# Performance work log

Measured on AMD Instinct MI355X. Metric: run time of the kernel, lower is better.

## Reference

```python
import jax, jax.numpy as jnp
import numpy as np

B, S, H, HF, V, L, NB, K = 8, 512, 1024, 512, 32000, 4, 8, 2
EPS = 1e-5


def _ln(x, g, b):
    m = jnp.mean(x, -1, keepdims=True)
    v = jnp.mean((x - m) ** 2, -1, keepdims=True)
    return (x - m) * jax.lax.rsqrt(v + EPS) * g + b


def setup_inputs() -> dict:
    key = jax.random.key(0)
    ks = jax.random.split(key, 12)
    n = lambda i, shape, s=0.02: jax.random.normal(ks[i], shape, jnp.float32) * s
    return {
        "input_ids": jax.random.randint(ks[0], (B, S), 0, V),
        "emb": n(1, (V, H)),
        "pos": n(2, (1, 512, H)),
        "torsion_field": jnp.zeros((1, H), jnp.float32),
        "lm_w": n(3, (H, V)),
        "lm_b": jnp.zeros((V,), jnp.float32),
        "sel_w": n(4, (L, H, NB)),
        "sel_b": jnp.zeros((L, NB), jnp.float32),
        "g1": jnp.ones((L, NB, H), jnp.float32),
        "b1": jnp.zeros((L, NB, H), jnp.float32),
        "attn_w": n(5, (L, NB, H, H)),
        "attn_b": jnp.zeros((L, NB, H), jnp.float32),
        "g2": jnp.ones((L, NB, H), jnp.float32),
        "b2": jnp.zeros((L, NB, H), jnp.float32),
        "ff1_w": n(6, (L, NB, H, HF)),
        "ff1_b": jnp.zeros((L, NB, HF), jnp.float32),
        "ff2_w": n(7, (L, NB, HF, H)),
        "ff2_b": jnp.zeros((L, NB, H), jnp.float32),
        "tg": n(8, (L, NB, H), 0.01),
    }


def _forward(input_ids, emb, pos, torsion_field, lm_w, lm_b, sel_w, sel_b,
             g1, b1, attn_w, attn_b, g2, b2, ff1_w, ff1_b, ff2_w, ff2_b, tg):
    # embedding + positional encoding
    h = emb[input_ids] + pos[:, :input_ids.shape[1], :]        # [B,S,H]
    tf = torsion_field[0]                                      # [H] (zeros buffer)
    PRIORITY = 0.5  # fresh block: success_rate*0.6 + excitement*0.4 = 0.5
    for l in range(L):
        # router: sigmoid(Linear(mean-pooled x)), mixed with block priority; topk on batch row 0
        scores = jax.nn.sigmoid(jnp.mean(h, 1) @ sel_w[l] + sel_b[l])   # [B,NB]
        adj0 = scores[0] * 0.7 + PRIORITY * 0.3                         # [NB]
        _, top_idx = jax.lax.top_k(adj0, K)                             # [K]
        params = jax.tree_util.tree_map(
            lambda p: p[l][top_idx],
            (g1, b1, attn_w, attn_b, g2, b2, ff1_w, ff1_b, ff2_w, ff2_b, tg))

        def blk(carry, p):
            pg1, pb1, pwa, pba, pg2, pb2, pw1, pbf1, pw2, pbf2, ptg = p
            x = carry
            ha = _ln(x, pg1, pb1) @ pwa + pba                           # [B,S,H]
            ha = ha * (1.0 + jax.nn.sigmoid(ptg) * tf)[None, None, :]
            hm = x + 0.5 * ha
            h2 = _ln(hm, pg2, pb2)
            h2 = jax.nn.gelu(h2 @ pw1 + pbf1, approximate=False) @ pw2 + pbf2
            return hm + 0.5 * h2, None

        h, _ = jax.lax.scan(blk, h, params)
        h = 1.5 * h  # h*0.5 + h after each layer
    return h @ lm_w + lm_b                                     # [B,S,V]


def reference(input_ids, emb, pos, torsion_field, lm_w, lm_b, sel_w, sel_b,
              g1, b1, attn_w, attn_b, g2, b2, ff1_w, ff1_b, ff2_w, ff2_b, tg):
    return _forward(input_ids, emb, pos, torsion_field, lm_w, lm_b, sel_w, sel_b,
                    g1, b1, attn_w, attn_b, g2, b2, ff1_w, ff1_b, ff2_w, ff2_b, tg)
```

## Files before the change

kernel.cpp:

```cpp
#include <hip/hip_runtime.h>


typedef unsigned short u16;
typedef short bf16x8 __attribute__((ext_vector_type(8)));
typedef float f32x4 __attribute__((ext_vector_type(4)));

struct __align__(8) u16x4_t { u16 x, y, z, w; };

#define MTOT 4096
#define HDIM 1024
#define HFF  512
#define VOC  32000
#define NLAYER 4
#define NBLK 8

#define VMW(n) asm volatile("s_waitcnt vmcnt(" #n ")" ::: "memory")
#define BARR() do { asm volatile("" ::: "memory"); __builtin_amdgcn_s_barrier(); asm volatile("" ::: "memory"); } while (0)

__device__ __forceinline__ u16 f2bf(float f) {
  unsigned u = __float_as_uint(f);
  unsigned r = u + 0x7FFFu + ((u >> 16) & 1u);
  return (u16)(r >> 16);
}

__device__ __forceinline__ float sigmoidf_(float z) {
  return 1.0f / (1.0f + expf(-z));
}

__device__ __forceinline__ void gload16(const void* g, void* l) {
  __builtin_amdgcn_global_load_lds(
      (const __attribute__((address_space(1))) void*)g,
      (__attribute__((address_space(3))) void*)l, 16, 0, 0);
}

__global__ void embed_lm_kernel(const int* __restrict__ ids,
                                const float* __restrict__ emb,
                                const float* __restrict__ pos,
                                float* __restrict__ x,
                                const float* __restrict__ lm_w,
                                u16* __restrict__ lmT) {
  __shared__ float tile[32][33];
  int b = blockIdx.x, tid = threadIdx.x;
  if (b < MTOT) {
    int s = b & 511;
    int id = ids[b];
    float4 e = ((const float4*)(emb + (size_t)id * HDIM))[tid];
    float4 p = ((const float4*)(pos + (size_t)s * HDIM))[tid];
    float4 r;
    r.x = e.x + p.x; r.y = e.y + p.y; r.z = e.z + p.z; r.w = e.w + p.w;
    ((float4*)(x + (size_t)b * HDIM))[tid] = r;
    return;
  }
  int c = b - MTOT;
  int n0 = (c % 1000) * 32, k0 = (c / 1000) * 32;
  int tx = tid & 31, ty = tid >> 5;
#pragma unroll
  for (int j = 0; j < 4; ++j) {
    int kr = k0 + ty + j * 8;
    tile[ty + j * 8][tx] = lm_w[(size_t)kr * VOC + n0 + tx];
  }
  __syncthreads();
#pragma unroll
  for (int j = 0; j < 4; ++j) {
    int nr = n0 + ty + j * 8;
    lmT[(size_t)nr * HDIM + k0 + tx] = f2bf(tile[tx][ty + j * 8]);
  }
}

__global__ void colsum_kernel(const float* __restrict__ x, float* __restrict__ partial) {
  int j = blockIdx.x;
  int t = threadIdx.x;
  float4 s; s.x = 0.f; s.y = 0.f; s.z = 0.f; s.w = 0.f;
  for (int r = 0; r < 8; ++r) {
    float4 a = ((const float4*)(x + (size_t)(j * 8 + r) * HDIM))[t];
    s.x += a.x; s.y += a.y; s.z += a.z; s.w += a.w;
  }
  ((float4*)(partial + (size_t)j * HDIM))[t] = s;
}

__global__ void router_finalize(const float* __restrict__ partial,
                                const float* __restrict__ selw,
                                const float* __restrict__ selb,
                                const float* __restrict__ tg_l,
                                const float* __restrict__ tf,
                                int* __restrict__ idx_out,
                                float* __restrict__ scale_out) {
  int t = threadIdx.x;
  float s = 0.f;
  for (int j = 0; j < 64; ++j) s += partial[(size_t)j * HDIM + t];
  float mean = s * (1.0f / 512.0f);
  __shared__ float sm[HDIM];
  __shared__ float sc[NBLK];
  __shared__ int sidx[2];
  sm[t] = mean;
  __syncthreads();
  int wave = t >> 6, lane = t & 63;
  if (wave < NBLK) {
    float p = 0.f;
    for (int h = lane; h < HDIM; h += 64) p += sm[h] * selw[h * NBLK + wave];
    for (int o = 32; o; o >>= 1) p += __shfl_down(p, o);
    if (lane == 0) sc[wave] = p;
  }
  __syncthreads();
  if (t == 0) {
    float adj[NBLK];
    for (int i = 0; i < NBLK; ++i) {
      float z = sc[i] + selb[i];
      adj[i] = sigmoidf_(z) * 0.7f + 0.15f;
    }
    int i0 = 0;
    for (int i = 1; i < NBLK; ++i) if (adj[i] > adj[i0]) i0 = i;
    int i1 = -1;
    for (int i = 0; i < NBLK; ++i) {
      if (i == i0) continue;
      if (i1 < 0 || adj[i] > adj[i1]) i1 = i;
    }
    idx_out[0] = i0; idx_out[1] = i1;
    sidx[0] = i0; sidx[1] = i1;
  }
  __syncthreads();
  for (int k = 0; k < 2; ++k) {
    int id = sidx[k];
    float z = tg_l[(size_t)id * HDIM + t];
    scale_out[k * HDIM + t] = 1.0f + sigmoidf_(z) * tf[t];
  }
}

__global__ void prep_kernel(const float* __restrict__ aw,
                            const float* __restrict__ f1w,
                            const float* __restrict__ f2w,
                            const int* __restrict__ idx, int slot,
                            u16* __restrict__ wA, u16* __restrict__ w1,
                            u16* __restrict__ w2,
                            const float* __restrict__ x,
                            const float* __restrict__ g_base,
                            const float* __restrict__ b_base,
                            u16* __restrict__ abf) {
  __shared__ float sh[32 * 33];
  int b = blockIdx.x, tid = threadIdx.x;
  int id = idx[slot];
  if (b < 2048) {
    float (*tile)[33] = (float(*)[33])sh;
    const float* src; u16* dst; int K, N, n0, k0;
    if (b < 1024) {
      K = 1024; N = 1024; src = aw + (size_t)id * 1024 * 1024;
      n0 = (b & 31) * 32; k0 = (b >> 5) * 32; dst = wA;
    } else if (b < 1536) {
      int c = b - 1024; K = 1024; N = 512; src = f1w + (size_t)id * 1024 * 512;
      n0 = (c & 15) * 32; k0 = (c >> 4) * 32; dst = w1;
    } else {
      int c = b - 1536; K = 512; N = 1024; src = f2w + (size_t)id * 512 * 1024;
      n0 = (c & 31) * 32; k0 = (c >> 5) * 32; dst = w2;
    }
    int tx = tid & 31, ty = tid >> 5;
#pragma unroll
    for (int j = 0; j < 4; ++j) {
      int kr = k0 + ty + j * 8;
      tile[ty + j * 8][tx] = src[(size_t)kr * N + n0 + tx];
    }
    __syncthreads();
#pragma unroll
    for (int j = 0; j < 4; ++j) {
      int nr = n0 + ty + j * 8;
      dst[(size_t)nr * K + k0 + tx] = f2bf(tile[tx][ty + j * 8]);
    }
    return;
  }
  int row = b - 2048, t = tid;
  const float* g = g_base + (size_t)id * HDIM;
  const float* bb = b_base + (size_t)id * HDIM;
  float4 v = ((const float4*)(x + (size_t)row * HDIM))[t];
  float s = v.x + v.y + v.z + v.w;
  float q = v.x * v.x + v.y * v.y + v.z * v.z + v.w * v.w;
  for (int o = 32; o; o >>= 1) { s += __shfl_down(s, o); q += __shfl_down(q, o); }
  float* ss = sh; float* sq = sh + 8;
  int wave = t >> 6, lane = t & 63;
  if (lane == 0) { ss[wave] = s; sq[wave] = q; }
  __syncthreads();
  if (t == 0) {
    float S = ss[0] + ss[1] + ss[2] + ss[3];
    float Q = sq[0] + sq[1] + sq[2] + sq[3];
    ss[0] = S * (1.0f / 1024.0f);
    sq[0] = Q * (1.0f / 1024.0f);
  }
  __syncthreads();
  float mean = ss[0];
  float var = sq[0] - mean * mean;
  float rs = rsqrtf(var + 1e-5f);
  float4 gv = ((const float4*)g)[t];
  float4 bv = ((const float4*)bb)[t];
  u16x4_t o4;
  o4.x = f2bf((v.x - mean) * rs * gv.x + bv.x);
  o4.y = f2bf((v.y - mean) * rs * gv.y + bv.y);
  o4.z = f2bf((v.z - mean) * rs * gv.z + bv.z);
  o4.w = f2bf((v.w - mean) * rs * gv.w + bv.w);
  ((u16x4_t*)(abf + (size_t)row * HDIM))[t] = o4;
}

__global__ void ln_kernel(const float* __restrict__ x,
                          const float* __restrict__ g_base,
                          const float* __restrict__ b_base,
                          const int* __restrict__ idx_ptr, int slot,
                          u16* __restrict__ out) {
  int row = blockIdx.x, t = threadIdx.x;
  size_t off = (size_t)idx_ptr[slot] * HDIM;
  const float* g = g_base + off;
  const float* b = b_base + off;
  float4 v = ((const float4*)(x + (size_t)row * HDIM))[t];
  float s = v.x + v.y + v.z + v.w;
  float q = v.x * v.x + v.y * v.y + v.z * v.z + v.w * v.w;
  for (int o = 32; o; o >>= 1) { s += __shfl_down(s, o); q += __shfl_down(q, o); }
  __shared__ float ss[4], sq[4];
  int wave = t >> 6, lane = t & 63;
  if (lane == 0) { ss[wave] = s; sq[wave] = q; }
  __syncthreads();
  if (t == 0) {
    float S = ss[0] + ss[1] + ss[2] + ss[3];
    float Q = sq[0] + sq[1] + sq[2] + sq[3];
    ss[0] = S * (1.0f / 1024.0f);
    sq[0] = Q * (1.0f / 1024.0f);
  }
  __syncthreads();
  float mean = ss[0];
  float var = sq[0] - mean * mean;
  float rs = rsqrtf(var + 1e-5f);
  float4 gv = ((const float4*)g)[t];
  float4 bv = ((const float4*)b)[t];
  u16x4_t o4;
  o4.x = f2bf((v.x - mean) * rs * gv.x + bv.x);
  o4.y = f2bf((v.y - mean) * rs * gv.y + bv.y);
  o4.z = f2bf((v.z - mean) * rs * gv.z + bv.z);
  o4.w = f2bf((v.w - mean) * rs * gv.w + bv.w);
  ((u16x4_t*)(out + (size_t)row * HDIM))[t] = o4;
}

template <int BM, int BN, int EPI>
__global__ __launch_bounds__(256) void gemm_layer(
    const u16* __restrict__ A, const u16* __restrict__ Bt, int N, int K,
    const float* __restrict__ bias_base, const int* __restrict__ idx_ptr,
    int slot, int bias_stride, const float* __restrict__ scale,
    float* __restrict__ xres, u16* __restrict__ outb, float lscale) {
  constexpr int TM = BM / 2, TN = BN / 2;
  constexpr int FM = TM / 16, FN = TN / 16;
  constexpr int NLD = (BM + BN) / 32;
  __shared__ __align__(16) u16 lds[(BM + BN) * 64];

  const int tid = threadIdx.x, wave = tid >> 6, lane = tid & 63;
  const int m0 = blockIdx.y * BM, n0 = blockIdx.x * BN;
  const int wm = wave >> 1, wn = wave & 1;
  const int fr = lane & 15, g = lane >> 4;
  const float* bias =
      bias_base + (idx_ptr ? (size_t)idx_ptr[slot] * bias_stride : 0);

  const u16* gbase[NLD];
  unsigned ldsoff[NLD];
#pragma unroll
  for (int j = 0; j < NLD; ++j) {
    int lo = (tid + j * 256) * 16;
    int q = (lo >> 4) & 7;
    if (lo < BM * 128) {
      int row = lo >> 7;
      gbase[j] = A + (size_t)(m0 + row) * K + (q ^ (row & 7)) * 8;
    } else {
      int bo = lo - BM * 128;
      int row = bo >> 7;
      gbase[j] = Bt + (size_t)(n0 + row) * K + (q ^ (row & 7)) * 8;
    }
    ldsoff[j] = (unsigned)(lo >> 1);
  }

  unsigned offA[FM][2], offB[FN][2];
#pragma unroll
  for (int mi = 0; mi < FM; ++mi)
#pragma unroll
    for (int kk = 0; kk < 2; ++kk)
      offA[mi][kk] = (unsigned)((wm * TM + mi * 16 + fr) * 128 +
                                (((kk * 4 + g) ^ (fr & 7)) << 4));
#pragma unroll
  for (int ni = 0; ni < FN; ++ni)
#pragma unroll
    for (int kk = 0; kk < 2; ++kk)
      offB[ni][kk] = (unsigned)(BM * 128 + (wn * TN + ni * 16 + fr) * 128 +
                                (((kk * 4 + g) ^ (fr & 7)) << 4));

  f32x4 acc[FM][FN];
#pragma unroll
  for (int i = 0; i < FM; ++i)
#pragma unroll
    for (int j = 0; j < FN; ++j) acc[i][j] = (f32x4){0.f, 0.f, 0.f, 0.f};

  for (int kt = 0; kt < K; kt += 64) {
#pragma unroll
    for (int j = 0; j < NLD; ++j) gload16(gbase[j] + kt, lds + ldsoff[j]);
    __syncthreads();
#pragma unroll
    for (int kk = 0; kk < 2; ++kk) {
      bf16x8 af[FM], bf[FN];
#pragma unroll
      for (int mi = 0; mi < FM; ++mi)
        af[mi] = *(const bf16x8*)((const char*)lds + offA[mi][kk]);
#pragma unroll
      for (int ni = 0; ni < FN; ++ni)
        bf[ni] = *(const bf16x8*)((const char*)lds + offB[ni][kk]);
#pragma unroll
      for (int mi = 0; mi < FM; ++mi)
#pragma unroll
        for (int ni = 0; ni < FN; ++ni)
          acc[mi][ni] = __builtin_amdgcn_mfma_f32_16x16x32_bf16(
              af[mi], bf[ni], acc[mi][ni], 0, 0, 0);
    }
    __syncthreads();
  }

  const int rb = g * 4, cn = fr;
  float bvv[FN], svv[FN];
#pragma unroll
  for (int ni = 0; ni < FN; ++ni) {
    int n = n0 + wn * TN + ni * 16 + cn;
    bvv[ni] = bias[n];
    svv[ni] = (EPI == 0) ? scale[n] : 0.f;
  }
#pragma unroll
  for (int mi = 0; mi < FM; ++mi) {
#pragma unroll
    for (int r = 0; r < 4; ++r) {
      int m = m0 + wm * TM + mi * 16 + rb + r;
      size_t base = (size_t)m * N + n0 + wn * TN + cn;
#pragma unroll
      for (int ni = 0; ni < FN; ++ni) {
        float c = acc[mi][ni][r] + bvv[ni];
        size_t o = base + ni * 16;
        if (EPI == 0) {
          xres[o] = xres[o] + 0.5f * (c * svv[ni]);
        } else if (EPI == 1) {
          float ge = 0.5f * c * (1.0f + erff(c * 0.70710678118654752f));
          outb[o] = f2bf(ge);
        } else if (EPI == 2) {
          xres[o] = (xres[o] + 0.5f * c) * lscale;
        } else {
          float v = (xres[o] + 0.5f * c) * lscale;
          xres[o] = v;
          outb[o] = f2bf(v);
        }
      }
    }
  }
}

__global__ __launch_bounds__(512, 2) void gemm_lm(
    const u16* __restrict__ A, const u16* __restrict__ Bt,
    const float* __restrict__ bias, float* __restrict__ out) {
  constexpr int K = HDIM;
  constexpr int N = VOC;
  constexpr int NT = K / 64;
  __shared__ __align__(16) u16 smbuf[2 * 32768];

  const int tid = threadIdx.x, wid = tid >> 6, lane = tid & 63;
  const int bid = blockIdx.x;
  const int vbid = (bid & 7) * 250 + (bid >> 3);
  const int n0 = (vbid >> 4) * 256;
  const int m0 = (vbid & 15) * 256;
  const int wm = wid >> 2, wn = wid & 3;
  const int fr = lane & 15, g = lane >> 4;

  const int r0 = tid >> 3, q = tid & 7;
  const int sg = (q ^ (r0 & 7)) * 8;
  const u16* usrc[4][2];
  unsigned uoff[4][2];
  usrc[0][0] = Bt + (size_t)(n0 + r0) * K + sg;        uoff[0][0] = 16384u + tid * 8;
  usrc[0][1] = Bt + (size_t)(n0 + 64 + r0) * K + sg;   uoff[0][1] = 20480u + tid * 8;
  usrc[1][0] = Bt + (size_t)(n0 + 128 + r0) * K + sg;  uoff[1][0] = 24576u + tid * 8;
  usrc[1][1] = Bt + (size_t)(n0 + 192 + r0) * K + sg;  uoff[1][1] = 28672u + tid * 8;
  usrc[2][0] = A + (size_t)(m0 + r0) * K + sg;         uoff[2][0] = 0u + tid * 8;
  usrc[2][1] = A + (size_t)(m0 + 128 + r0) * K + sg;   uoff[2][1] = 8192u + tid * 8;
  usrc[3][0] = A + (size_t)(m0 + 64 + r0) * K + sg;    uoff[3][0] = 4096u + tid * 8;
  usrc[3][1] = A + (size_t)(m0 + 192 + r0) * K + sg;   uoff[3][1] = 12288u + tid * 8;

  unsigned offA[8][2], offB[4][2];
#pragma unroll
  for (int mi = 0; mi < 8; ++mi)
#pragma unroll
    for (int kk = 0; kk < 2; ++kk)
      offA[mi][kk] = (unsigned)((wm * 128 + mi * 16 + fr) * 128 +
                                (((kk * 4 + g) ^ (fr & 7)) << 4));
#pragma unroll
  for (int ni = 0; ni < 4; ++ni)
#pragma unroll
    for (int kk = 0; kk < 2; ++kk)
      offB[ni][kk] = (unsigned)(32768 + (wn * 64 + ni * 16 + fr) * 128 +
                                (((kk * 4 + g) ^ (fr & 7)) << 4));

  f32x4 acc[8][4];
#pragma unroll
  for (int i = 0; i < 8; ++i)
#pragma unroll
    for (int j = 0; j < 4; ++j) acc[i][j] = (f32x4){0.f, 0.f, 0.f, 0.f};

#pragma unroll
  for (int u = 0; u < 4; ++u) {
    gload16(usrc[u][0], smbuf + uoff[u][0]);
    gload16(usrc[u][1], smbuf + uoff[u][1]);
  }

  for (int t = 0; t < NT; ++t) {
    const char* cb = (const char*)smbuf + (size_t)(t & 1) * 65536;
    u16* nb = smbuf + ((t + 1) & 1) * 32768;
    const int ko = (t + 1) * 64;
    const bool st = (t + 1 < NT);
    bf16x8 avl[4], avh[4], bv[4];
    VMW(2);
    BARR();
#pragma unroll
    for (int ni = 0; ni < 4; ++ni) bv[ni] = *(const bf16x8*)(cb + offB[ni][0]);
#pragma unroll
    for (int mi = 0; mi < 4; ++mi) avl[mi] = *(const bf16x8*)(cb + offA[mi][0]);
    if (st) {
      gload16(usrc[0][0] + ko, nb + uoff[0][0]);
      gload16(usrc[0][1] + ko, nb + uoff[0][1]);
    }
    __builtin_amdgcn_s_setprio(1);
#pragma unroll
    for (int mi = 0; mi < 4; ++mi)
#pragma unroll
      for (int ni = 0; ni < 4; ++ni)
        acc[mi][ni] = __builtin_amdgcn_mfma_f32_16x16x32_bf16(
            avl[mi], bv[ni], acc[mi][ni], 0, 0, 0);
    __builtin_amdgcn_s_setprio(0);
    if (t < NT - 1) { VMW(2); } else { VMW(0); }
    BARR();
#pragma unroll
    for (int mi = 0; mi < 4; ++mi)
      avh[mi] = *(const bf16x8*)(cb + offA[4 + mi][0]);
    if (st) {
      gload16(usrc[1][0] + ko, nb + uoff[1][0]);
      gload16(usrc[1][1] + ko, nb + uoff[1][1]);
    }
    __builtin_amdgcn_s_setprio(1);
#pragma unroll
    for (int mi = 0; mi < 4; ++mi)
#pragma unroll
      for (int ni = 0; ni < 4; ++ni)
        acc[4 + mi][ni] = __builtin_amdgcn_mfma_f32_16x16x32_bf16(
            avh[mi], bv[ni], acc[4 + mi][ni], 0, 0, 0);
    __builtin_amdgcn_s_setprio(0);
#pragma unroll
    for (int ni = 0; ni < 4; ++ni) bv[ni] = *(const bf16x8*)(cb + offB[ni][1]);
#pragma unroll
    for (int mi = 0; mi < 4; ++mi) avl[mi] = *(const bf16x8*)(cb + offA[mi][1]);
    if (st) {
      gload16(usrc[2][0] + ko, nb + uoff[2][0]);
      gload16(usrc[2][1] + ko, nb + uoff[2][1]);
    }
    __builtin_amdgcn_s_setprio(1);
#pragma unroll
    for (int mi = 0; mi < 4; ++mi)
#pragma unroll
      for (int ni = 0; ni < 4; ++ni)
        acc[mi][ni] = __builtin_amdgcn_mfma_f32_16x16x32_bf16(
            avl[mi], bv[ni], acc[mi][ni], 0, 0, 0);
    __builtin_amdgcn_s_setprio(0);
#pragma unroll
    for (int mi = 0; mi < 4; ++mi)
      avh[mi] = *(const bf16x8*)(cb + offA[4 + mi][1]);
    if (st) {
      gload16(usrc[3][0] + ko, nb + uoff[3][0]);
      gload16(usrc[3][1] + ko, nb + uoff[3][1]);
    }
    __builtin_amdgcn_s_setprio(1);
#pragma unroll
    for (int mi = 0; mi < 4; ++mi)
#pragma unroll
      for (int ni = 0; ni < 4; ++ni)
        acc[4 + mi][ni] = __builtin_amdgcn_mfma_f32_16x16x32_bf16(
            avh[mi], bv[ni], acc[4 + mi][ni], 0, 0, 0);
    __builtin_amdgcn_s_setprio(0);
  }

  const int rb = g * 4, cn = fr;
  float bvv[4];
#pragma unroll
  for (int ni = 0; ni < 4; ++ni) bvv[ni] = bias[n0 + wn * 64 + ni * 16 + cn];
#pragma unroll
  for (int mi = 0; mi < 8; ++mi) {
#pragma unroll
    for (int r = 0; r < 4; ++r) {
      int m = m0 + wm * 128 + mi * 16 + rb + r;
      float* orow = out + (size_t)m * N + n0 + wn * 64 + cn;
#pragma unroll
      for (int ni = 0; ni < 4; ++ni)
        __builtin_nontemporal_store(acc[mi][ni][r] + bvv[ni], orow + ni * 16);
    }
  }
}

extern "C" void kernel_launch(void* const* d_in, const int* in_sizes, int n_in,
                              void* d_out, int out_size, void* d_ws,
                              size_t ws_size, hipStream_t stream) {
  (void)in_sizes; (void)n_in; (void)out_size; (void)ws_size;
  const int*   ids    = (const int*)d_in[0];
  const float* emb    = (const float*)d_in[1];
  const float* pos    = (const float*)d_in[2];
  const float* tf     = (const float*)d_in[3];
  const float* lm_w   = (const float*)d_in[4];
  const float* lm_b   = (const float*)d_in[5];
  const float* sel_w  = (const float*)d_in[6];
  const float* sel_b  = (const float*)d_in[7];
  const float* g1     = (const float*)d_in[8];
  const float* b1     = (const float*)d_in[9];
  const float* attn_w = (const float*)d_in[10];
  const float* attn_b = (const float*)d_in[11];
  const float* g2     = (const float*)d_in[12];
  const float* b2     = (const float*)d_in[13];
  const float* ff1_w  = (const float*)d_in[14];
  const float* ff1_b  = (const float*)d_in[15];
  const float* ff2_w  = (const float*)d_in[16];
  const float* ff2_b  = (const float*)d_in[17];
  const float* tg     = (const float*)d_in[18];
  float* out = (float*)d_out;

  char* ws = (char*)d_ws;
  float* x       = (float*)(ws + 0);
  u16*   abf     = (u16*)(ws + 16777216);
  u16*   tbuf    = (u16*)(ws + 25165824);
  u16*   wA      = (u16*)(ws + 29360128);
  u16*   w1      = (u16*)(ws + 31457280);
  u16*   w2      = (u16*)(ws + 32505856);
  u16*   lmT     = (u16*)(ws + 33554432);
  float* partial = (float*)(ws + 99090432);
  float* scalev  = (float*)(ws + 99352576);
  int*   idx     = (int*)(ws + 99360768);

  embed_lm_kernel<<<MTOT + VOC, 256, 0, stream>>>(ids, emb, pos, x, lm_w, lmT);

  for (int l = 0; l < NLAYER; ++l) {
    colsum_kernel<<<64, 256, 0, stream>>>(x, partial);
    router_finalize<<<1, 1024, 0, stream>>>(
        partial, sel_w + (size_t)l * HDIM * NBLK, sel_b + l * NBLK,
        tg + (size_t)l * NBLK * HDIM, tf, idx, scalev);
    const float* aw_l  = attn_w + (size_t)l * NBLK * HDIM * HDIM;
    const float* f1w_l = ff1_w + (size_t)l * NBLK * HDIM * HFF;
    const float* f2w_l = ff2_w + (size_t)l * NBLK * HFF * HDIM;
    for (int k = 0; k < 2; ++k) {
      prep_kernel<<<2048 + MTOT, 256, 0, stream>>>(
          aw_l, f1w_l, f2w_l, idx, k, wA, w1, w2, x,
          g1 + (size_t)l * NBLK * HDIM, b1 + (size_t)l * NBLK * HDIM, abf);
      gemm_layer<128, 64, 0><<<dim3(16, 32), 256, 0, stream>>>(
          abf, wA, HDIM, HDIM, attn_b + (size_t)l * NBLK * HDIM, idx, k, HDIM,
          scalev + k * HDIM, x, nullptr, 1.0f);
      ln_kernel<<<MTOT, 256, 0, stream>>>(x, g2 + (size_t)l * NBLK * HDIM,
                                          b2 + (size_t)l * NBLK * HDIM, idx, k,
                                          abf);
      gemm_layer<64, 64, 1><<<dim3(8, 64), 256, 0, stream>>>(
          abf, w1, HFF, HDIM, ff1_b + (size_t)l * NBLK * HFF, idx, k, HFF,
          nullptr, nullptr, tbuf, 1.0f);
      float lsc = (k == 1) ? 1.5f : 1.0f;
      if (l == NLAYER - 1 && k == 1) {
        gemm_layer<128, 64, 3><<<dim3(16, 32), 256, 0, stream>>>(
            tbuf, w2, HDIM, HFF, ff2_b + (size_t)l * NBLK * HDIM, idx, k, HDIM,
            nullptr, x, abf, lsc);
      } else {
        gemm_layer<128, 64, 2><<<dim3(16, 32), 256, 0, stream>>>(
            tbuf, w2, HDIM, HFF, ff2_b + (size_t)l * NBLK * HDIM, idx, k, HDIM,
            nullptr, x, nullptr, lsc);
      }
    }
  }

  gemm_lm<<<2000, 512, 0, stream>>>(abf, lmT, lm_b, out);
}
```

Measured before the change: 977.7 us.

## Unroll LM-head GEMM K loop by two with barrier-per-quarter ping-pong schedule

Restructures the LM-head GEMM main loop to process two K tiles per iteration with fixed double-buffer addresses. It adds a barrier around every MFMA quarter so waves alternate between LDS reads plus global issue and MFMA bursts, in a ping-pong style. MFMAs are reordered so consecutive instructions use different accumulators, which reduces back-to-back dependency stalls. The cost is many more barriers per K tile, and the waitcnt placement changes, which risks synchronisation overhead or subtle correctness issues around buffer reuse.

```diff
diff --git a/kernel.cpp b/kernel.cpp
--- a/kernel.cpp
+++ b/kernel.cpp
@@ -347,12 +347,26 @@
   }
 }
 
+#define MFMA_Q(ACCBASE, AV0, AV1, AV2, AV3)                                   \
+  __builtin_amdgcn_s_setprio(1);                                              \
+  _Pragma("unroll")                                                           \
+  for (int ni = 0; ni < 4; ++ni) {                                            \
+    acc[ACCBASE + 0][ni] = __builtin_amdgcn_mfma_f32_16x16x32_bf16(           \
+        AV0, bv[ni], acc[ACCBASE + 0][ni], 0, 0, 0);                          \
+    acc[ACCBASE + 1][ni] = __builtin_amdgcn_mfma_f32_16x16x32_bf16(           \
+        AV1, bv[ni], acc[ACCBASE + 1][ni], 0, 0, 0);                          \
+    acc[ACCBASE + 2][ni] = __builtin_amdgcn_mfma_f32_16x16x32_bf16(           \
+        AV2, bv[ni], acc[ACCBASE + 2][ni], 0, 0, 0);                          \
+    acc[ACCBASE + 3][ni] = __builtin_amdgcn_mfma_f32_16x16x32_bf16(           \
+        AV3, bv[ni], acc[ACCBASE + 3][ni], 0, 0, 0);                          \
+  }                                                                           \
+  __builtin_amdgcn_s_setprio(0);
+
 __global__ __launch_bounds__(512, 2) void gemm_lm(
     const u16* __restrict__ A, const u16* __restrict__ Bt,
     const float* __restrict__ bias, float* __restrict__ out) {
   constexpr int K = HDIM;
   constexpr int N = VOC;
-  constexpr int NT = K / 64;
   __shared__ __align__(16) u16 smbuf[2 * 32768];
 
   const int tid = threadIdx.x, wid = tid >> 6, lane = tid & 63;
@@ -401,79 +415,113 @@
     gload16(usrc[u][0], smbuf + uoff[u][0]);
     gload16(usrc[u][1], smbuf + uoff[u][1]);
   }
-
-  for (int t = 0; t < NT; ++t) {
-    const char* cb = (const char*)smbuf + (size_t)(t & 1) * 65536;
-    u16* nb = smbuf + ((t + 1) & 1) * 32768;
-    const int ko = (t + 1) * 64;
-    const bool st = (t + 1 < NT);
-    bf16x8 avl[4], avh[4], bv[4];
+  VMW(2);
+  BARR();
+
+  for (int it = 0; it < 8; ++it) {
+    const char* c0 = (const char*)smbuf;
+    const char* c1 = (const char*)smbuf + 65536;
+    u16* s0 = smbuf;
+    u16* s1 = smbuf + 32768;
+    const int k1 = (2 * it + 1) * 64;
+    const int k2 = (2 * it + 2) * 64;
+    const bool st2 = (it < 7);
+    bf16x8 bv[4], a0, a1, a2, a3;
+
+#pragma unroll
+    for (int ni = 0; ni < 4; ++ni) bv[ni] = *(const bf16x8*)(c0 + offB[ni][0]);
+    a0 = *(const bf16x8*)(c0 + offA[0][0]);
+    a1 = *(const bf16x8*)(c0 + offA[1][0]);
+    a2 = *(const bf16x8*)(c0 + offA[2][0]);
+    a3 = *(const bf16x8*)(c0 + offA[3][0]);
+    gload16(usrc[0][0] + k1, s1 + uoff[0][0]);
+    gload16(usrc[0][1] + k1, s1 + uoff[0][1]);
     VMW(2);
     BARR();
-#pragma unroll
-    for (int ni = 0; ni < 4; ++ni) bv[ni] = *(const bf16x8*)(cb + offB[ni][0]);
-#pragma unroll
-    for (int mi = 0; mi < 4; ++mi) avl[mi] = *(const bf16x8*)(cb + offA[mi][0]);
-    if (st) {
-      gload16(usrc[0][0] + ko, nb + uoff[0][0]);
-      gload16(usrc[0][1] + ko, nb + uoff[0][1]);
-    }
-    __builtin_amdgcn_s_setprio(1);
-#pragma unroll
-    for (int mi = 0; mi < 4; ++mi)
-#pragma unroll
-      for (int ni = 0; ni < 4; ++ni)
-        acc[mi][ni] = __builtin_amdgcn_mfma_f32_16x16x32_bf16(
-            avl[mi], bv[ni], acc[mi][ni], 0, 0, 0);
-    __builtin_amdgcn_s_setprio(0);
-    if (t < NT - 1) { VMW(2); } else { VMW(0); }
-    BARR();
-#pragma unroll
-    for (int mi = 0; mi < 4; ++mi)
-      avh[mi] = *(const bf16x8*)(cb + offA[4 + mi][0]);
-    if (st) {
-      gload16(usrc[1][0] + ko, nb + uoff[1][0]);
-      gload16(usrc[1][1] + ko, nb + uoff[1][1]);
-    }
-    __builtin_amdgcn_s_setprio(1);
-#pragma unroll
-    for (int mi = 0; mi < 4; ++mi)
-#pragma unroll
-      for (int ni = 0; ni < 4; ++ni)
-        acc[4 + mi][ni] = __builtin_amdgcn_mfma_f32_16x16x32_bf16(
-            avh[mi], bv[ni], acc[4 + mi][ni], 0, 0, 0);
-    __builtin_amdgcn_s_setprio(0);
-#pragma unroll
-    for (int ni = 0; ni < 4; ++ni) bv[ni] = *(const bf16x8*)(cb + offB[ni][1]);
-#pragma unroll
-    for (int mi = 0; mi < 4; ++mi) avl[mi] = *(const bf16x8*)(cb + offA[mi][1]);
-    if (st) {
-      gload16(usrc[2][0] + ko, nb + uoff[2][0]);
-      gload16(usrc[2][1] + ko, nb + uoff[2][1]);
-    }
-    __builtin_amdgcn_s_setprio(1);
-#pragma unroll
-    for (int mi = 0; mi < 4; ++mi)
-#pragma unroll
-      for (int ni = 0; ni < 4; ++ni)
-        acc[mi][ni] = __builtin_amdgcn_mfma_f32_16x16x32_bf16(
-            avl[mi], bv[ni], acc[mi][ni], 0, 0, 0);
-    __builtin_amdgcn_s_setprio(0);
-#pragma unroll
-    for (int mi = 0; mi < 4; ++mi)
-      avh[mi] = *(const bf16x8*)(cb + offA[4 + mi][1]);
-    if (st) {
-      gload16(usrc[3][0] + ko, nb + uoff[3][0]);
-      gload16(usrc[3][1] + ko, nb + uoff[3][1]);
-    }
-    __builtin_amdgcn_s_setprio(1);
-#pragma unroll
-    for (int mi = 0; mi < 4; ++mi)
-#pragma unroll
-      for (int ni = 0; ni < 4; ++ni)
-        acc[4 + mi][ni] = __builtin_amdgcn_mfma_f32_16x16x32_bf16(
-            avh[mi], bv[ni], acc[4 + mi][ni], 0, 0, 0);
-    __builtin_amdgcn_s_setprio(0);
+    MFMA_Q(0, a0, a1, a2, a3);
+    BARR();
+    a0 = *(const bf16x8*)(c0 + offA[4][0]);
+    a1 = *(const bf16x8*)(c0 + offA[5][0]);
+    a2 = *(const bf16x8*)(c0 + offA[6][0]);
+    a3 = *(const bf16x8*)(c0 + offA[7][0]);
+    gload16(usrc[1][0] + k1, s1 + uoff[1][0]);
+    gload16(usrc[1][1] + k1, s1 + uoff[1][1]);
+    BARR();
+    MFMA_Q(4, a0, a1, a2, a3);
+    BARR();
+#pragma unroll
+    for (int ni = 0; ni < 4; ++ni) bv[ni] = *(const bf16x8*)(c0 + offB[ni][1]);
+    a0 = *(const bf16x8*)(c0 + offA[0][1]);
+    a1 = *(const bf16x8*)(c0 + offA[1][1]);
+    a2 = *(const bf16x8*)(c0 + offA[2][1]);
+    a3 = *(const bf16x8*)(c0 + offA[3][1]);
+    gload16(usrc[2][0] + k1, s1 + uoff[2][0]);
+    gload16(usrc[2][1] + k1, s1 + uoff[2][1]);
+    BARR();
+    MFMA_Q(0, a0, a1, a2, a3);
+    BARR();
+    a0 = *(const bf16x8*)(c0 + offA[4][1]);
+    a1 = *(const bf16x8*)(c0 + offA[5][1]);
+    a2 = *(const bf16x8*)(c0 + offA[6][1]);
+    a3 = *(const bf16x8*)(c0 + offA[7][1]);
+    gload16(usrc[3][0] + k1, s1 + uoff[3][0]);
+    gload16(usrc[3][1] + k1, s1 + uoff[3][1]);
+    VMW(2);
+    BARR();
+    MFMA_Q(4, a0, a1, a2, a3);
+    BARR();
+#pragma unroll
+    for (int ni = 0; ni < 4; ++ni) bv[ni] = *(const bf16x8*)(c1 + offB[ni][0]);
+    a0 = *(const bf16x8*)(c1 + offA[0][0]);
+    a1 = *(const bf16x8*)(c1 + offA[1][0]);
+    a2 = *(const bf16x8*)(c1 + offA[2][0]);
+    a3 = *(const bf16x8*)(c1 + offA[3][0]);
+    if (st2) {
+      gload16(usrc[0][0] + k2, s0 + uoff[0][0]);
+      gload16(usrc[0][1] + k2, s0 + uoff[0][1]);
+      VMW(2);
+    } else {
+      VMW(0);
+    }
+    BARR();
+    MFMA_Q(0, a0, a1, a2, a3);
+    BARR();
+    a0 = *(const bf16x8*)(c1 + offA[4][0]);
+    a1 = *(const bf16x8*)(c1 + offA[5][0]);
+    a2 = *(const bf16x8*)(c1 + offA[6][0]);
+    a3 = *(const bf16x8*)(c1 + offA[7][0]);
+    if (st2) {
+      gload16(usrc[1][0] + k2, s0 + uoff[1][0]);
+      gload16(usrc[1][1] + k2, s0 + uoff[1][1]);
+    }
+    BARR();
+    MFMA_Q(4, a0, a1, a2, a3);
+    BARR();
+#pragma unroll
+    for (int ni = 0; ni < 4; ++ni) bv[ni] = *(const bf16x8*)(c1 + offB[ni][1]);
+    a0 = *(const bf16x8*)(c1 + offA[0][1]);
+    a1 = *(const bf16x8*)(c1 + offA[1][1]);
+    a2 = *(const bf16x8*)(c1 + offA[2][1]);
+    a3 = *(const bf16x8*)(c1 + offA[3][1]);
+    if (st2) {
+      gload16(usrc[2][0] + k2, s0 + uoff[2][0]);
+      gload16(usrc[2][1] + k2, s0 + uoff[2][1]);
+    }
+    BARR();
+    MFMA_Q(0, a0, a1, a2, a3);
+    BARR();
+    a0 = *(const bf16x8*)(c1 + offA[4][1]);
+    a1 = *(const bf16x8*)(c1 + offA[5][1]);
+    a2 = *(const bf16x8*)(c1 + offA[6][1]);
+    a3 = *(const bf16x8*)(c1 + offA[7][1]);
+    if (st2) {
+      gload16(usrc[3][0] + k2, s0 + uoff[3][0]);
+      gload16(usrc[3][1] + k2, s0 + uoff[3][1]);
+      VMW(2);
+    }
+    BARR();
+    MFMA_Q(4, a0, a1, a2, a3);
+    BARR();
   }
 
   const int rb = g * 4, cn = fr;
```

New measurement: 980.8 us. Within noise of the previous version (+0.3%).
